# Kernel optimization log

Measured on AMD Instinct MI355X. Metric: run time of the kernel, lower is better.

Reference implementation:

```python
import jax, jax.numpy as jnp
import numpy as np

B, TAPE, N, F = 128, 100000, 50000, 32

def setup_inputs() -> dict:
    key = jax.random.key(0)
    k1, k2, k3, k4 = jax.random.split(key, 4)
    tape = jax.random.normal(k1, (B, TAPE), dtype=jnp.float32)
    input_indices = jax.random.randint(k2, (N, F), 0, TAPE)
    # He init scaled by fan-in, padding slots (index==0) zeroed as in __init__
    weights = jax.random.normal(k3, (N, F), dtype=jnp.float32) * jnp.sqrt(2.0 / F)
    weights = jnp.where(input_indices == 0, 0.0, weights)
    bias = jnp.zeros((N,), dtype=jnp.float32)
    output_indices = jnp.arange(N)
    act_type = jax.random.randint(k4, (N,), 0, 2)
    return {"tape": tape, "weights": weights, "bias": bias,
            "input_indices": input_indices, "output_indices": output_indices,
            "act_type": act_type}

def reference(tape, weights, bias, input_indices, output_indices, act_type):
    # gather padded fan-in inputs: [B, N, F]
    gathered = tape[:, input_indices]
    # weighted sum over fan-in + bias: [B, N]
    x = jnp.einsum('bnf,nf->bn', gathered, weights) + bias
    # per-activation-type apply (two activation groups: relu / tanh)
    x = jnp.where(act_type == 0, jax.nn.relu(x), jnp.tanh(x))
    # scatter results back into tape
    return tape.at[:, output_indices].set(x)
```

## Files before the change

### kernel.cpp

```cpp
#include <hip/hip_runtime.h>
#include <cmath>

#define TAPE_SZ 100000
#define N_SZ    50000
#define F_SZ    32
#define B_SZ    128
#define NGRP    8
#define GSUB    16
#define NBV     64
#define NCHUNK  ((N_SZ + NBV - 1) / NBV)
#define NGATHER (NCHUNK * NGRP)
#define NTAIL   512
#define TAIL_F4 1600000

static __device__ __forceinline__ unsigned short f32_to_bf16(float f) {
    unsigned int u = __float_as_uint(f);
    u = (u + 0x7fffu + ((u >> 16) & 1u)) >> 16;
    return (unsigned short)u;
}

__global__ __launch_bounds__(256) void transpose_tape(const float* __restrict__ in,
                                                      unsigned short* __restrict__ outT) {
    __shared__ float tile[32][129];
    const int x0 = blockIdx.x * 32;
    const int tx = threadIdx.x;
    const int ty = threadIdx.y;

    #pragma unroll
    for (int yy = ty; yy < B_SZ; yy += 8)
        tile[tx][yy] = in[(size_t)yy * TAPE_SZ + x0 + tx];
    __syncthreads();

    const int tid = ty * 32 + tx;
    const int g = tid >> 5;
    const int l = tid & 31;
    unsigned short* dst = outT + ((size_t)g * TAPE_SZ + x0 + l) * GSUB;
    union { unsigned short u[8]; uint4 q; } p0, p1;
    #pragma unroll
    for (int k = 0; k < 8; ++k) {
        p0.u[k] = f32_to_bf16(tile[l][g * GSUB + k]);
        p1.u[k] = f32_to_bf16(tile[l][g * GSUB + 8 + k]);
    }
    *(uint4*)dst       = p0.q;
    *(uint4*)(dst + 8) = p1.q;
}

__global__ __launch_bounds__(256, 8) void gather_mm(const unsigned short* __restrict__ tapeT,
                                                    const float* __restrict__ weights,
                                                    const float* __restrict__ bias,
                                                    const int*   __restrict__ in_idx,
                                                    const int*   __restrict__ out_idx,
                                                    const int*   __restrict__ act_type,
                                                    const float* __restrict__ tape,
                                                    float* __restrict__ out) {
    __shared__ int2  s_iw[NBV][33];
    __shared__ float s_bias[NBV];
    __shared__ int   s_act[NBV];
    __shared__ int   s_oidx[NBV];
    float (*s_x)[68] = (float (*)[68])&s_iw[0][0];

    const int tid = threadIdx.x;

    if (blockIdx.x >= NGATHER) {
        const float4* src = (const float4*)tape;
        float4*       dst = (float4*)out;
        const int stride = NTAIL * 256;
        for (int i = (blockIdx.x - NGATHER) * 256 + tid; i < TAIL_F4; i += stride) {
            const int b = i / 12500;
            const int j = i - b * 12500;
            const int off = b * (TAPE_SZ / 4) + (N_SZ / 4) + j;
            dst[off] = src[off];
        }
        return;
    }

    const int g     = blockIdx.x & (NGRP - 1);
    const int chunk = blockIdx.x >> 3;
    const int n0    = chunk * NBV;
    const int nend  = min(NBV, N_SZ - n0);

    for (int t = tid; t < nend * 32; t += 256) {
        const int n = t >> 5, f = t & 31;
        s_iw[n][f] = make_int2(in_idx[(size_t)n0 * 32 + t],
                               __float_as_int(weights[(size_t)n0 * 32 + t]));
    }
    if (tid < nend) {
        s_bias[tid] = bias[n0 + tid];
        s_act[tid]  = act_type[n0 + tid];
        s_oidx[tid] = out_idx[n0 + tid];
    }
    __syncthreads();

    const int nl = tid >> 2;
    const int q  = tid & 3;
    const unsigned short* tg = tapeT + (size_t)g * TAPE_SZ * GSUB + q * 4;

    float a0 = 0.f, a1 = 0.f, a2 = 0.f, a3 = 0.f;
    if (nl < nend) {
        #pragma unroll
        for (int fo = 0; fo < 32; fo += 8) {
            int2 iw8[8];
            #pragma unroll
            for (int j = 0; j < 8; ++j) iw8[j] = s_iw[nl][fo + j];
            uint2 q8[8];
            #pragma unroll
            for (int j = 0; j < 8; ++j)
                q8[j] = *(const uint2*)(tg + (size_t)iw8[j].x * GSUB);
            #pragma unroll
            for (int j = 0; j < 8; ++j) {
                const float w = __int_as_float(iw8[j].y);
                a0 = fmaf(__uint_as_float(q8[j].x << 16),         w, a0);
                a1 = fmaf(__uint_as_float(q8[j].x & 0xffff0000u), w, a1);
                a2 = fmaf(__uint_as_float(q8[j].y << 16),         w, a2);
                a3 = fmaf(__uint_as_float(q8[j].y & 0xffff0000u), w, a3);
            }
        }
        const float bz = s_bias[nl];
        a0 += bz; a1 += bz; a2 += bz; a3 += bz;
        if (s_act[nl] == 0) {
            a0 = fmaxf(a0, 0.f); a1 = fmaxf(a1, 0.f);
            a2 = fmaxf(a2, 0.f); a3 = fmaxf(a3, 0.f);
        } else {
            a0 = tanhf(a0); a1 = tanhf(a1); a2 = tanhf(a2); a3 = tanhf(a3);
        }
    }
    __syncthreads();

    if (nl < nend) {
        const int bs = q * 4;
        s_x[bs + 0][nl] = a0; s_x[bs + 1][nl] = a1;
        s_x[bs + 2][nl] = a2; s_x[bs + 3][nl] = a3;
    }
    __syncthreads();

    const int quads = (nend + 3) >> 2;
    for (int idx = tid; idx < GSUB * quads; idx += 256) {
        int bsub, j4;
        if (nend == NBV) { bsub = idx >> 4; j4 = idx & 15; }
        else             { bsub = idx / quads; j4 = idx - bsub * quads; }
        const int nq  = j4 * 4;
        const int oc0 = s_oidx[nq];
        float* orow = out + (size_t)(g * GSUB + bsub) * TAPE_SZ;
        const bool consec = (nq + 3 < nend) &&
                            (s_oidx[nq + 1] == oc0 + 1) &&
                            (s_oidx[nq + 2] == oc0 + 2) &&
                            (s_oidx[nq + 3] == oc0 + 3) && ((oc0 & 3) == 0);
        if (consec) {
            *(float4*)(orow + oc0) = make_float4(s_x[bsub][nq + 0], s_x[bsub][nq + 1],
                                                 s_x[bsub][nq + 2], s_x[bsub][nq + 3]);
        } else {
            #pragma unroll
            for (int c = 0; c < 4; ++c)
                if (nq + c < nend) orow[s_oidx[nq + c]] = s_x[bsub][nq + c];
        }
    }
}

__global__ __launch_bounds__(128) void gather_fallback(const float* __restrict__ tape,
                                                       const float* __restrict__ weights,
                                                       const float* __restrict__ bias,
                                                       const int*   __restrict__ in_idx,
                                                       const int*   __restrict__ out_idx,
                                                       const int*   __restrict__ act_type,
                                                       float* __restrict__ out) {
    const int n = blockIdx.x;
    const int b = threadIdx.x;
    float acc = 0.f;
    for (int f = 0; f < F_SZ; ++f) {
        acc += tape[(size_t)b * TAPE_SZ + in_idx[(size_t)n * F_SZ + f]] *
               weights[(size_t)n * F_SZ + f];
    }
    acc += bias[n];
    acc = (act_type[n] == 0) ? fmaxf(acc, 0.f) : tanhf(acc);
    out[(size_t)b * TAPE_SZ + out_idx[n]] = acc;
}

__global__ __launch_bounds__(256) void copy_tail_fb(const float* __restrict__ tape,
                                                    float* __restrict__ out) {
    const int n4 = (TAPE_SZ - N_SZ) / 4;
    int i = blockIdx.x * blockDim.x + threadIdx.x;
    int b = blockIdx.y;
    if (i < n4) {
        const float4* src = (const float4*)(tape + (size_t)b * TAPE_SZ + N_SZ);
        float4*       dst = (float4*)(out  + (size_t)b * TAPE_SZ + N_SZ);
        dst[i] = src[i];
    }
}

extern "C" void kernel_launch(void* const* d_in, const int* in_sizes, int n_in,
                              void* d_out, int out_size, void* d_ws, size_t ws_size,
                              hipStream_t stream) {
    const float* tape    = (const float*)d_in[0];
    const float* weights = (const float*)d_in[1];
    const float* bias    = (const float*)d_in[2];
    const int*   in_idx  = (const int*)d_in[3];
    const int*   out_idx = (const int*)d_in[4];
    const int*   act     = (const int*)d_in[5];
    float*       out     = (float*)d_out;

    const size_t need = (size_t)TAPE_SZ * B_SZ * sizeof(unsigned short);
    if (ws_size >= need) {
        unsigned short* tapeT = (unsigned short*)d_ws;
        transpose_tape<<<dim3(TAPE_SZ / 32), dim3(32, 8), 0, stream>>>(tape, tapeT);
        gather_mm<<<dim3(NGATHER + NTAIL), dim3(256), 0, stream>>>(
            tapeT, weights, bias, in_idx, out_idx, act, tape, out);
    } else {
        copy_tail_fb<<<dim3(((TAPE_SZ - N_SZ) / 4 + 255) / 256, B_SZ), 256, 0, stream>>>(tape, out);
        gather_fallback<<<dim3(N_SZ), 128, 0, stream>>>(
            tape, weights, bias, in_idx, out_idx, act, out);
    }
}
```

Before: 187.8 us.

## Split gather into two tape-half passes with 32-batch bf16 groups

Re-layouts the bf16 transposed tape into 4 groups of 32 batch entries so each gather loads 64 bytes (uint4) per index, and fuses the tail copy into the transpose kernel. The gather is split into two launches, one per half of the tape index range, so each pass touches a smaller working set that may fit in cache. Partial sums pass between the launches through an fp32 workspace buffer. This adds an extra kernel launch, the write and re-read of the partial sums, and predicated loads that waste lanes.

Result: slower. 204.4 us (+8.9%).

```diff
diff --git a/kernel.cpp b/kernel.cpp
--- a/kernel.cpp
+++ b/kernel.cpp
@@ -5,13 +5,12 @@
 #define N_SZ    50000
 #define F_SZ    32
 #define B_SZ    128
-#define NGRP    8
-#define GSUB    16
+#define GSUB    32
+#define NGRP    4
+#define HSPLIT  50000
 #define NBV     64
 #define NCHUNK  ((N_SZ + NBV - 1) / NBV)
-#define NGATHER (NCHUNK * NGRP)
-#define NTAIL   512
-#define TAIL_F4 1600000
+#define GRID_G  ((NCHUNK / 2) * 8)
 
 static __device__ __forceinline__ unsigned short f32_to_bf16(float f) {
     unsigned int u = __float_as_uint(f);
@@ -19,8 +18,9 @@
     return (unsigned short)u;
 }
 
-__global__ __launch_bounds__(256) void transpose_tape(const float* __restrict__ in,
-                                                      unsigned short* __restrict__ outT) {
+__global__ __launch_bounds__(256) void transpose_g32(const float* __restrict__ in,
+                                                     unsigned short* __restrict__ outG,
+                                                     float* __restrict__ out) {
     __shared__ float tile[32][129];
     const int x0 = blockIdx.x * 32;
     const int tx = threadIdx.x;
@@ -32,126 +32,151 @@
     __syncthreads();
 
     const int tid = ty * 32 + tx;
-    const int g = tid >> 5;
-    const int l = tid & 31;
-    unsigned short* dst = outT + ((size_t)g * TAPE_SZ + x0 + l) * GSUB;
+    const int l = tid >> 3;
+    const int o = tid & 7;
+    const int g = o >> 1;
+    const int hf = o & 1;
+    unsigned short* dst = outG + ((size_t)g * TAPE_SZ + x0 + l) * GSUB + hf * 16;
     union { unsigned short u[8]; uint4 q; } p0, p1;
     #pragma unroll
     for (int k = 0; k < 8; ++k) {
-        p0.u[k] = f32_to_bf16(tile[l][g * GSUB + k]);
-        p1.u[k] = f32_to_bf16(tile[l][g * GSUB + 8 + k]);
+        p0.u[k] = f32_to_bf16(tile[l][g * GSUB + hf * 16 + k]);
+        p1.u[k] = f32_to_bf16(tile[l][g * GSUB + hf * 16 + 8 + k]);
     }
     *(uint4*)dst       = p0.q;
     *(uint4*)(dst + 8) = p1.q;
-}
-
-__global__ __launch_bounds__(256, 8) void gather_mm(const unsigned short* __restrict__ tapeT,
-                                                    const float* __restrict__ weights,
-                                                    const float* __restrict__ bias,
-                                                    const int*   __restrict__ in_idx,
-                                                    const int*   __restrict__ out_idx,
-                                                    const int*   __restrict__ act_type,
-                                                    const float* __restrict__ tape,
-                                                    float* __restrict__ out) {
-    __shared__ int2  s_iw[NBV][33];
+
+    if (x0 + tx >= N_SZ) {
+        #pragma unroll
+        for (int yy = ty; yy < B_SZ; yy += 8)
+            out[(size_t)yy * TAPE_SZ + x0 + tx] = tile[tx][yy];
+    }
+}
+
+template<int HALF>
+__global__ __launch_bounds__(256) void gather_h(
+    const unsigned short* __restrict__ tapeG,
+    const float* __restrict__ weights,
+    const float* __restrict__ bias,
+    const int*   __restrict__ in_idx,
+    const int*   __restrict__ out_idx,
+    const int*   __restrict__ act_type,
+    float* __restrict__ acc,
+    float* __restrict__ out) {
+    __shared__ union {
+        int2  iw[NBV][33];
+        float x[GSUB][66];
+    } u;
     __shared__ float s_bias[NBV];
     __shared__ int   s_act[NBV];
     __shared__ int   s_oidx[NBV];
-    float (*s_x)[68] = (float (*)[68])&s_iw[0][0];
-
-    const int tid = threadIdx.x;
-
-    if (blockIdx.x >= NGATHER) {
-        const float4* src = (const float4*)tape;
-        float4*       dst = (float4*)out;
-        const int stride = NTAIL * 256;
-        for (int i = (blockIdx.x - NGATHER) * 256 + tid; i < TAIL_F4; i += stride) {
-            const int b = i / 12500;
-            const int j = i - b * 12500;
-            const int off = b * (TAPE_SZ / 4) + (N_SZ / 4) + j;
-            dst[off] = src[off];
-        }
-        return;
-    }
-
-    const int g     = blockIdx.x & (NGRP - 1);
-    const int chunk = blockIdx.x >> 3;
+
+    const int tid   = threadIdx.x;
+    const int i     = blockIdx.x;
+    const int g     = i & 3;
+    const int sub   = (i >> 2) & 1;
+    const int chunk = (i >> 3) * 2 + sub;
     const int n0    = chunk * NBV;
     const int nend  = min(NBV, N_SZ - n0);
 
     for (int t = tid; t < nend * 32; t += 256) {
         const int n = t >> 5, f = t & 31;
-        s_iw[n][f] = make_int2(in_idx[(size_t)n0 * 32 + t],
+        u.iw[n][f] = make_int2(in_idx[(size_t)n0 * 32 + t],
                                __float_as_int(weights[(size_t)n0 * 32 + t]));
     }
-    if (tid < nend) {
+    if (HALF == 1 && tid < nend) {
         s_bias[tid] = bias[n0 + tid];
         s_act[tid]  = act_type[n0 + tid];
         s_oidx[tid] = out_idx[n0 + tid];
     }
     __syncthreads();
 
-    const int nl = tid >> 2;
-    const int q  = tid & 3;
-    const unsigned short* tg = tapeT + (size_t)g * TAPE_SZ * GSUB + q * 4;
-
-    float a0 = 0.f, a1 = 0.f, a2 = 0.f, a3 = 0.f;
-    if (nl < nend) {
-        #pragma unroll
-        for (int fo = 0; fo < 32; fo += 8) {
-            int2 iw8[8];
-            #pragma unroll
-            for (int j = 0; j < 8; ++j) iw8[j] = s_iw[nl][fo + j];
-            uint2 q8[8];
-            #pragma unroll
-            for (int j = 0; j < 8; ++j)
-                q8[j] = *(const uint2*)(tg + (size_t)iw8[j].x * GSUB);
-            #pragma unroll
-            for (int j = 0; j < 8; ++j) {
-                const float w = __int_as_float(iw8[j].y);
-                a0 = fmaf(__uint_as_float(q8[j].x << 16),         w, a0);
-                a1 = fmaf(__uint_as_float(q8[j].x & 0xffff0000u), w, a1);
-                a2 = fmaf(__uint_as_float(q8[j].y << 16),         w, a2);
-                a3 = fmaf(__uint_as_float(q8[j].y & 0xffff0000u), w, a3);
-            }
-        }
+    const int nl  = tid >> 2;
+    const int seg = tid & 3;
+    const bool an = (nl < nend);
+    const unsigned short* tg = tapeG + (size_t)g * TAPE_SZ * GSUB + seg * 8;
+
+    float a[8];
+    #pragma unroll
+    for (int k = 0; k < 8; ++k) a[k] = 0.f;
+
+    #pragma unroll
+    for (int fo = 0; fo < 32; fo += 8) {
+        int r8[8]; float w8[8];
+        #pragma unroll
+        for (int j = 0; j < 8; ++j) {
+            const int2 iw = u.iw[nl][fo + j];
+            r8[j] = iw.x; w8[j] = __int_as_float(iw.y);
+        }
+        uint4 q8[8];
+        #pragma unroll
+        for (int j = 0; j < 8; ++j) {
+            q8[j] = make_uint4(0u, 0u, 0u, 0u);
+            const bool c = an && (HALF == 0 ? (r8[j] < HSPLIT) : (r8[j] >= HSPLIT));
+            if (c) q8[j] = *(const uint4*)(tg + (size_t)r8[j] * GSUB);
+        }
+        #pragma unroll
+        for (int j = 0; j < 8; ++j) {
+            const float wv = w8[j];
+            a[0] = fmaf(__uint_as_float(q8[j].x << 16),         wv, a[0]);
+            a[1] = fmaf(__uint_as_float(q8[j].x & 0xffff0000u), wv, a[1]);
+            a[2] = fmaf(__uint_as_float(q8[j].y << 16),         wv, a[2]);
+            a[3] = fmaf(__uint_as_float(q8[j].y & 0xffff0000u), wv, a[3]);
+            a[4] = fmaf(__uint_as_float(q8[j].z << 16),         wv, a[4]);
+            a[5] = fmaf(__uint_as_float(q8[j].z & 0xffff0000u), wv, a[5]);
+            a[6] = fmaf(__uint_as_float(q8[j].w << 16),         wv, a[6]);
+            a[7] = fmaf(__uint_as_float(q8[j].w & 0xffff0000u), wv, a[7]);
+        }
+    }
+
+    float* ap = acc + (size_t)(n0 + nl) * B_SZ + g * GSUB + seg * 8;
+    if (HALF == 0) {
+        if (an) {
+            *(float4*)(ap)     = make_float4(a[0], a[1], a[2], a[3]);
+            *(float4*)(ap + 4) = make_float4(a[4], a[5], a[6], a[7]);
+        }
+        return;
+    }
+
+    if (an) {
+        const float4 p0 = *(const float4*)(ap);
+        const float4 p1 = *(const float4*)(ap + 4);
+        a[0] += p0.x; a[1] += p0.y; a[2] += p0.z; a[3] += p0.w;
+        a[4] += p1.x; a[5] += p1.y; a[6] += p1.z; a[7] += p1.w;
         const float bz = s_bias[nl];
-        a0 += bz; a1 += bz; a2 += bz; a3 += bz;
-        if (s_act[nl] == 0) {
-            a0 = fmaxf(a0, 0.f); a1 = fmaxf(a1, 0.f);
-            a2 = fmaxf(a2, 0.f); a3 = fmaxf(a3, 0.f);
-        } else {
-            a0 = tanhf(a0); a1 = tanhf(a1); a2 = tanhf(a2); a3 = tanhf(a3);
-        }
-    }
-    __syncthreads();
-
-    if (nl < nend) {
-        const int bs = q * 4;
-        s_x[bs + 0][nl] = a0; s_x[bs + 1][nl] = a1;
-        s_x[bs + 2][nl] = a2; s_x[bs + 3][nl] = a3;
+        const int   at = s_act[nl];
+        #pragma unroll
+        for (int k = 0; k < 8; ++k) {
+            const float v = a[k] + bz;
+            a[k] = (at == 0) ? fmaxf(v, 0.f) : tanhf(v);
+        }
+    }
+    __syncthreads();
+    if (an) {
+        #pragma unroll
+        for (int k = 0; k < 8; ++k) u.x[seg * 8 + k][nl] = a[k];
     }
     __syncthreads();
 
     const int quads = (nend + 3) >> 2;
-    for (int idx = tid; idx < GSUB * quads; idx += 256) {
-        int bsub, j4;
-        if (nend == NBV) { bsub = idx >> 4; j4 = idx & 15; }
-        else             { bsub = idx / quads; j4 = idx - bsub * quads; }
+    for (int it = tid; it < GSUB * quads; it += 256) {
+        int bl, j4;
+        if (nend == NBV) { bl = it >> 4; j4 = it & 15; }
+        else             { bl = it / quads; j4 = it - bl * quads; }
         const int nq  = j4 * 4;
         const int oc0 = s_oidx[nq];
-        float* orow = out + (size_t)(g * GSUB + bsub) * TAPE_SZ;
+        float* orow = out + (size_t)(g * GSUB + bl) * TAPE_SZ;
         const bool consec = (nq + 3 < nend) &&
                             (s_oidx[nq + 1] == oc0 + 1) &&
                             (s_oidx[nq + 2] == oc0 + 2) &&
                             (s_oidx[nq + 3] == oc0 + 3) && ((oc0 & 3) == 0);
         if (consec) {
-            *(float4*)(orow + oc0) = make_float4(s_x[bsub][nq + 0], s_x[bsub][nq + 1],
-                                                 s_x[bsub][nq + 2], s_x[bsub][nq + 3]);
+            *(float4*)(orow + oc0) = make_float4(u.x[bl][nq + 0], u.x[bl][nq + 1],
+                                                 u.x[bl][nq + 2], u.x[bl][nq + 3]);
         } else {
             #pragma unroll
             for (int c = 0; c < 4; ++c)
-                if (nq + c < nend) orow[s_oidx[nq + c]] = s_x[bsub][nq + c];
+                if (nq + c < nend) orow[s_oidx[nq + c]] = u.x[bl][nq + c];
         }
     }
 }
@@ -198,12 +223,15 @@
     const int*   act     = (const int*)d_in[5];
     float*       out     = (float*)d_out;
 
-    const size_t need = (size_t)TAPE_SZ * B_SZ * sizeof(unsigned short);
-    if (ws_size >= need) {
-        unsigned short* tapeT = (unsigned short*)d_ws;
-        transpose_tape<<<dim3(TAPE_SZ / 32), dim3(32, 8), 0, stream>>>(tape, tapeT);
-        gather_mm<<<dim3(NGATHER + NTAIL), dim3(256), 0, stream>>>(
-            tapeT, weights, bias, in_idx, out_idx, act, tape, out);
+    const size_t one = (size_t)TAPE_SZ * B_SZ * sizeof(unsigned short);
+    if (ws_size >= 2 * one) {
+        unsigned short* tapeG = (unsigned short*)d_ws;
+        float*          accp  = (float*)((char*)d_ws + one);
+        transpose_g32<<<dim3(TAPE_SZ / 32), dim3(32, 8), 0, stream>>>(tape, tapeG, out);
+        gather_h<0><<<dim3(GRID_G), dim3(256), 0, stream>>>(
+            tapeG, weights, bias, in_idx, out_idx, act, accp, out);
+        gather_h<1><<<dim3(GRID_G), dim3(256), 0, stream>>>(
+            tapeG, weights, bias, in_idx, out_idx, act, accp, out);
     } else {
         copy_tail_fb<<<dim3(((TAPE_SZ - N_SZ) / 4 + 255) / 256, B_SZ), 256, 0, stream>>>(tape, out);
         gather_fallback<<<dim3(N_SZ), 128, 0, stream>>>(
```
